# Performance work log

Hardware: AMD Instinct MI355X
Metric: run time of the kernel (lower is better)

The kernel has to match this reference:

```python
import jax, jax.numpy as jnp
import numpy as np

R = 16
ALPHA = 32.0
SCALING = ALPHA / R


def setup_inputs() -> dict:
    key = jax.random.key(0)
    ks = jax.random.split(key, 6)
    B, T, C, O, E = 16, 1500, 1024, 1024, 8
    x = jax.random.normal(ks[0], (B, T, C), dtype=jnp.float32)
    # gate weights per batch element (e.g. softmax-like, but module accepts any)
    w = jax.random.uniform(ks[1], (B, E), dtype=jnp.float32)
    W_base = jax.random.normal(ks[2], (O, C), dtype=jnp.float32) * 0.02
    b_base = jax.random.normal(ks[3], (O,), dtype=jnp.float32) * 0.02
    As = jax.random.normal(ks[4], (E, R, C), dtype=jnp.float32) * 0.02
    Bs = jax.random.normal(ks[5], (E, O, R), dtype=jnp.float32) * 0.02
    return {"x": x, "w": w, "W_base": W_base, "b_base": b_base, "As": As, "Bs": Bs}


def reference(x, w, W_base, b_base, As, Bs):
    # base linear: (B,T,C) @ (C,O) + b
    out = jnp.einsum('btc,oc->bto', x, W_base) + b_base
    # per-expert low-rank: h[b,t,e,r] = x[b,t,:] @ A_e^T
    h = jnp.einsum('btc,erc->bter', x, As)          # (B,T,E,R)
    # y[b,t,e,o] = h @ B_e^T ; gate-weighted sum over experts
    lora = jnp.einsum('bter,eor,be->bto', h, Bs, w)  # (B,T,O)
    return out + lora * SCALING
```

## Files before the change

kernel.cpp:

```cpp
#include <hip/hip_runtime.h>
#include <stdint.h>
#include <stddef.h>


#define B_ 16
#define T_ 1500
#define C_ 1024
#define O_ 1024
#define E_ 8
#define R_ 16
#define ER 128
#define KK 1152
#define BT 24000
#define NKT 18
#define SCALING 2.0f

typedef __bf16 bf16x8 __attribute__((ext_vector_type(8)));
typedef float f32x4 __attribute__((ext_vector_type(4)));
typedef unsigned short u16;
typedef u16 u16x8 __attribute__((ext_vector_type(8)));

__device__ inline u16 f2bf(float f) {
  union { float f; unsigned u; } v; v.f = f;
  unsigned u = v.u;
  u += 0x7fff + ((u >> 16) & 1);
  return (u16)(u >> 16);
}

#define GLL(gp, lp)                                                            \
  __builtin_amdgcn_global_load_lds(                                            \
      (const __attribute__((address_space(1))) void*)(gp),                     \
      (__attribute__((address_space(3))) void*)(lp), 16, 0, 0)

#define SBAR __builtin_amdgcn_sched_barrier(0)

__global__ __launch_bounds__(256) void prep_w(const float* __restrict__ Wb,
                                              const float* __restrict__ Bs,
                                              const float* __restrict__ As,
                                              u16* __restrict__ wp,
                                              u16* __restrict__ ap) {
  int idx = blockIdx.x * 256 + threadIdx.x;
  if (idx < O_ * KK) {
    int o = idx / KK;
    int k = idx - o * KK;
    float v;
    if (k < C_) {
      v = Wb[o * C_ + k];
    } else {
      int j = k - C_;
      v = Bs[((j >> 4) * O_ + o) * R_ + (j & 15)];
    }
    wp[idx] = f2bf(v);
  } else {
    int a = idx - O_ * KK;
    ap[a] = f2bf(As[a]);
  }
}

__global__ __launch_bounds__(256) void cvt(const float* __restrict__ x,
                                           u16* __restrict__ xp) {
  const int t0 = blockIdx.x * 256 + threadIdx.x;
#pragma unroll
  for (int u = 0; u < 6; ++u) {
    const int chunk = u * 512000 + t0;
    const int row = chunk >> 7;
    const int cc = (chunk & 127) * 8;
    const float4 v0 = *(const float4*)&x[(size_t)row * C_ + cc];
    const float4 v1 = *(const float4*)&x[(size_t)row * C_ + cc + 4];
    u16x8 o;
    o[0] = f2bf(v0.x); o[1] = f2bf(v0.y); o[2] = f2bf(v0.z); o[3] = f2bf(v0.w);
    o[4] = f2bf(v1.x); o[5] = f2bf(v1.y); o[6] = f2bf(v1.z); o[7] = f2bf(v1.w);
    *(u16x8*)&xp[(size_t)row * KK + cc] = o;
  }
}

__global__ __launch_bounds__(256) void h_gemm(const u16* __restrict__ xp,
                                              const u16* __restrict__ ab,
                                              const float* __restrict__ w,
                                              u16* __restrict__ xpo) {
  const int mt = blockIdx.x;
  const int tid = threadIdx.x, lane = tid & 63, wv = tid >> 6;
  const int wrow = wv & 1, wcol = wv >> 1, l15 = lane & 15, quad = lane >> 4;
  const int s7 = l15 & 7;

  __shared__ u16 lA[64 * 64];
  __shared__ u16 lB[128 * 64];

  const u16* gA = xp + (size_t)mt * 64 * KK;

  f32x4 acc[2][4];
#pragma unroll
  for (int i = 0; i < 2; ++i)
#pragma unroll
    for (int j = 0; j < 4; ++j) acc[i][j] = (f32x4){0.f, 0.f, 0.f, 0.f};

  int arow[2], ako[2], brow[4], bko[4];
#pragma unroll
  for (int c = 0; c < 2; ++c) {
    int idx = c * 256 + tid;
    arow[c] = idx >> 3;
    ako[c] = (((idx & 7) ^ (arow[c] & 7)) << 3);
  }
#pragma unroll
  for (int c = 0; c < 4; ++c) {
    int idx = c * 256 + tid;
    brow[c] = idx >> 3;
    bko[c] = (((idx & 7) ^ (brow[c] & 7)) << 3);
  }

  for (int kt = 0; kt < C_ / 64; ++kt) {
    const int k0 = kt * 64;
#pragma unroll
    for (int c = 0; c < 2; ++c)
      GLL(gA + (size_t)arow[c] * KK + k0 + ako[c], &lA[(c * 256 + tid) * 8]);
#pragma unroll
    for (int c = 0; c < 4; ++c)
      GLL(ab + brow[c] * C_ + k0 + bko[c], &lB[(c * 256 + tid) * 8]);
    __syncthreads();
#pragma unroll
    for (int kk = 0; kk < 2; ++kk) {
      const int ko = (((kk * 4 + quad) ^ s7) << 3);
      bf16x8 af[2], bfr[4];
#pragma unroll
      for (int i = 0; i < 2; ++i)
        af[i] = *(const bf16x8*)&lA[(wrow * 32 + i * 16 + l15) * 64 + ko];
#pragma unroll
      for (int j = 0; j < 4; ++j)
        bfr[j] = *(const bf16x8*)&lB[(wcol * 64 + j * 16 + l15) * 64 + ko];
#pragma unroll
      for (int i = 0; i < 2; ++i)
#pragma unroll
        for (int j = 0; j < 4; ++j)
          acc[i][j] = __builtin_amdgcn_mfma_f32_16x16x32_bf16(af[i], bfr[j], acc[i][j], 0, 0, 0);
    }
    __syncthreads();
  }

#pragma unroll
  for (int j = 0; j < 4; ++j) {
    const int col = wcol * 64 + j * 16 + l15;
    const int e = wcol * 4 + j;
#pragma unroll
    for (int i = 0; i < 2; ++i) {
#pragma unroll
      for (int rr = 0; rr < 4; ++rr) {
        const int row = mt * 64 + wrow * 32 + i * 16 + quad * 4 + rr;
        const int b = row / T_;
        xpo[(size_t)row * KK + C_ + col] = f2bf(acc[i][j][rr] * (SCALING * w[b * E_ + e]));
      }
    }
  }
}

__global__ __launch_bounds__(512, 2) void main_gemm(const u16* __restrict__ xp,
                                                    const u16* __restrict__ wp,
                                                    const float* __restrict__ bb,
                                                    float* __restrict__ out) {
  const int id = blockIdx.x;
  const int xcd = id & 7, win = id >> 3;
  const int g = (xcd < 4 ? xcd * 63 : 252 + (xcd - 4) * 62) + win;
  const int mt = g >> 2;
  const int nt = g & 3;
  const int tid = threadIdx.x, lane = tid & 63, wv = tid >> 6;
  const int wm = wv >> 2, wn = wv & 3, l15 = lane & 15, quad = lane >> 4;
  const int s7 = l15 & 7;
  const int ko0 = (quad ^ s7) << 3;
  const int ko1 = ((4 + quad) ^ s7) << 3;

  __shared__ u16 lA[2][192 * 64];
  __shared__ u16 lB[2][256 * 64];

  const u16* gA = xp + (size_t)mt * 192 * KK;
  const u16* gB = wp + (size_t)nt * 256 * KK;

  f32x4 acc[6][4];
#pragma unroll
  for (int i = 0; i < 6; ++i)
#pragma unroll
    for (int j = 0; j < 4; ++j) acc[i][j] = (f32x4){0.f, 0.f, 0.f, 0.f};

  const u16* pA[3];
  const u16* pB[4];
  int dA[3], dB[4];
#pragma unroll
  for (int c = 0; c < 3; ++c) {
    int idx = c * 512 + tid;
    int row = idx >> 3;
    pA[c] = gA + (size_t)row * KK + (((idx & 7) ^ (row & 7)) << 3);
    dA[c] = idx * 8;
  }
#pragma unroll
  for (int c = 0; c < 4; ++c) {
    int idx = c * 512 + tid;
    int row = idx >> 3;
    pB[c] = gB + (size_t)row * KK + (((idx & 7) ^ (row & 7)) << 3);
    dB[c] = idx * 8;
  }

#define ROWA(i) ((wm * 96 + (i) * 16 + l15) * 64)
#define ROWB(j) ((wn * 64 + (j) * 16 + l15) * 64)

#pragma unroll
  for (int c = 0; c < 3; ++c) GLL(pA[c], &lA[0][dA[c]]);
#pragma unroll
  for (int c = 0; c < 4; ++c) GLL(pB[c], &lB[0][dB[c]]);
#pragma unroll
  for (int c = 0; c < 3; ++c) GLL(pA[c] + 64, &lA[1][dA[c]]);
#pragma unroll
  for (int c = 0; c < 4; ++c) GLL(pB[c] + 64, &lB[1][dB[c]]);
  asm volatile("s_waitcnt vmcnt(7)" ::: "memory");
  SBAR;
  __builtin_amdgcn_s_barrier();
  SBAR;

  bf16x8 af0[3][2], af1[3][2], bfA[4][2], bfB[4][2];
#pragma unroll
  for (int i = 0; i < 3; ++i) {
    af0[i][0] = *(const bf16x8*)&lA[0][ROWA(i) + ko0];
    af0[i][1] = *(const bf16x8*)&lA[0][ROWA(i) + ko1];
  }
#pragma unroll
  for (int j = 0; j < 4; ++j) {
    bfA[j][0] = *(const bf16x8*)&lB[0][ROWB(j) + ko0];
    bfA[j][1] = *(const bf16x8*)&lB[0][ROWB(j) + ko1];
  }

#define TILE_BODY(T, CUR, BC, BN_)                                             \
  {                                                                            \
    const int t_ = (T);                                                        \
    _Pragma("unroll")                                                          \
    for (int i = 0; i < 3; ++i) {                                              \
      af1[i][0] = *(const bf16x8*)&lA[CUR][ROWA(i + 3) + ko0];                 \
      af1[i][1] = *(const bf16x8*)&lA[CUR][ROWA(i + 3) + ko1];                 \
    }                                                                          \
    __builtin_amdgcn_s_setprio(1);                                             \
    _Pragma("unroll")                                                          \
    for (int ks = 0; ks < 2; ++ks)                                             \
      _Pragma("unroll")                                                        \
      for (int i = 0; i < 3; ++i)                                              \
        _Pragma("unroll")                                                      \
        for (int j = 0; j < 4; ++j)                                            \
          acc[i][j] = __builtin_amdgcn_mfma_f32_16x16x32_bf16(                 \
              af0[i][ks], BC[j][ks], acc[i][j], 0, 0, 0);                      \
    __builtin_amdgcn_s_setprio(0);                                             \
    asm volatile("s_waitcnt lgkmcnt(0)" ::: "memory");                         \
    SBAR;                                                                      \
    __builtin_amdgcn_s_barrier();               \
    SBAR;                                                                      \
    if (t_ + 2 < NKT) {                                                        \
      const int k2 = (t_ + 2) * 64;                                            \
      _Pragma("unroll")                                                        \
      for (int c = 0; c < 3; ++c) GLL(pA[c] + k2, &lA[CUR][dA[c]]);            \
      _Pragma("unroll")                                                        \
      for (int c = 0; c < 4; ++c) GLL(pB[c] + k2, &lB[CUR][dB[c]]);            \
      asm volatile("s_waitcnt vmcnt(7)" ::: "memory");                         \
    } else {                                                                   \
      asm volatile("s_waitcnt vmcnt(0)" ::: "memory");                         \
    }                                                                          \
    SBAR;                                                                      \
    __builtin_amdgcn_s_barrier();     \
    SBAR;                                                                      \
    if (t_ + 1 < NKT) {                                                        \
      _Pragma("unroll")                                                        \
      for (int i = 0; i < 3; ++i) {                                            \
        af0[i][0] = *(const bf16x8*)&lA[CUR ^ 1][ROWA(i) + ko0];               \
        af0[i][1] = *(const bf16x8*)&lA[CUR ^ 1][ROWA(i) + ko1];               \
      }                                                                        \
      _Pragma("unroll")                                                        \
      for (int j = 0; j < 4; ++j) {                                            \
        BN_[j][0] = *(const bf16x8*)&lB[CUR ^ 1][ROWB(j) + ko0];               \
        BN_[j][1] = *(const bf16x8*)&lB[CUR ^ 1][ROWB(j) + ko1];               \
      }                                                                        \
    }                                                                          \
    __builtin_amdgcn_s_setprio(1);                                             \
    _Pragma("unroll")                                                          \
    for (int ks = 0; ks < 2; ++ks)                                             \
      _Pragma("unroll")                                                        \
      for (int i = 0; i < 3; ++i)                                              \
        _Pragma("unroll")                                                      \
        for (int j = 0; j < 4; ++j)                                            \
          acc[i + 3][j] = __builtin_amdgcn_mfma_f32_16x16x32_bf16(             \
              af1[i][ks], BC[j][ks], acc[i + 3][j], 0, 0, 0);                  \
    __builtin_amdgcn_s_setprio(0);                                             \
  }

  for (int tt = 0; tt < 9; ++tt) {
    TILE_BODY(2 * tt, 0, bfA, bfB)
    TILE_BODY(2 * tt + 1, 1, bfB, bfA)
  }
#undef TILE_BODY
#undef ROWA
#undef ROWB

#pragma unroll
  for (int j = 0; j < 4; ++j) {
    const int col = nt * 256 + wn * 64 + j * 16 + l15;
    const float bias = bb[col];
#pragma unroll
    for (int i = 0; i < 6; ++i) {
#pragma unroll
      for (int rr = 0; rr < 4; ++rr) {
        const int row = mt * 192 + wm * 96 + i * 16 + quad * 4 + rr;
        out[(size_t)row * O_ + col] = acc[i][j][rr] + bias;
      }
    }
  }
}

extern "C" void kernel_launch(void* const* d_in, const int* in_sizes, int n_in,
                              void* d_out, int out_size, void* d_ws, size_t ws_size,
                              hipStream_t stream) {
  const float* x = (const float*)d_in[0];
  const float* w = (const float*)d_in[1];
  const float* Wb = (const float*)d_in[2];
  const float* bb = (const float*)d_in[3];
  const float* As = (const float*)d_in[4];
  const float* Bs = (const float*)d_in[5];
  float* out = (float*)d_out;

  u16* xp = (u16*)d_ws;
  u16* wp = xp + (size_t)BT * KK;
  u16* ap = wp + (size_t)O_ * KK;

  prep_w<<<(O_ * KK + ER * C_) / 256, 256, 0, stream>>>(Wb, Bs, As, wp, ap);
  cvt<<<2000, 256, 0, stream>>>(x, xp);
  h_gemm<<<375, 256, 0, stream>>>(xp, ap, w, xp);
  main_gemm<<<500, 512, 0, stream>>>(xp, wp, bb, out);
}
```

Measured before the change: 275.4 us.

## Shrink main GEMM tile to 128 rows and use a triple-buffered LDS pipeline

The main GEMM tile shrinks from 192x256 to 128x256, which raises the grid from 500 to 752 blocks and adds a row guard on the output store. Shared memory is now triple-buffered: each k-step issues the global-to-LDS loads for two steps ahead, then reads this step's fragments in staged LDS reads interleaved with partial MFMA groups through lgkmcnt waits. The goal is to hide load latency with fewer barriers per step and to balance work across CUs. The cost is lower arithmetic intensity per block and more LDS use (about 144KB), which limits the kernel to one block per CU.

```diff
diff --git a/kernel.cpp b/kernel.cpp
--- a/kernel.cpp
+++ b/kernel.cpp
@@ -157,8 +157,7 @@
                                                     const float* __restrict__ bb,
                                                     float* __restrict__ out) {
   const int id = blockIdx.x;
-  const int xcd = id & 7, win = id >> 3;
-  const int g = (xcd < 4 ? xcd * 63 : 252 + (xcd - 4) * 62) + win;
+  const int g = (id & 7) * 94 + (id >> 3);
   const int mt = g >> 2;
   const int nt = g & 3;
   const int tid = threadIdx.x, lane = tid & 63, wv = tid >> 6;
@@ -167,23 +166,23 @@
   const int ko0 = (quad ^ s7) << 3;
   const int ko1 = ((4 + quad) ^ s7) << 3;
 
-  __shared__ u16 lA[2][192 * 64];
-  __shared__ u16 lB[2][256 * 64];
-
-  const u16* gA = xp + (size_t)mt * 192 * KK;
+  __shared__ u16 lA[3][128 * 64];
+  __shared__ u16 lB[3][256 * 64];
+
+  const u16* gA = xp + (size_t)mt * 128 * KK;
   const u16* gB = wp + (size_t)nt * 256 * KK;
 
-  f32x4 acc[6][4];
-#pragma unroll
-  for (int i = 0; i < 6; ++i)
+  f32x4 acc[4][4];
+#pragma unroll
+  for (int i = 0; i < 4; ++i)
 #pragma unroll
     for (int j = 0; j < 4; ++j) acc[i][j] = (f32x4){0.f, 0.f, 0.f, 0.f};
 
-  const u16* pA[3];
+  const u16* pA[2];
   const u16* pB[4];
-  int dA[3], dB[4];
-#pragma unroll
-  for (int c = 0; c < 3; ++c) {
+  int dA[2], dB[4];
+#pragma unroll
+  for (int c = 0; c < 2; ++c) {
     int idx = c * 512 + tid;
     int row = idx >> 3;
     pA[c] = gA + (size_t)row * KK + (((idx & 7) ^ (row & 7)) << 3);
@@ -197,96 +196,105 @@
     dB[c] = idx * 8;
   }
 
-#define ROWA(i) ((wm * 96 + (i) * 16 + l15) * 64)
+#define ROWA(i) ((wm * 64 + (i) * 16 + l15) * 64)
 #define ROWB(j) ((wn * 64 + (j) * 16 + l15) * 64)
 
 #pragma unroll
-  for (int c = 0; c < 3; ++c) GLL(pA[c], &lA[0][dA[c]]);
+  for (int c = 0; c < 2; ++c) GLL(pA[c], &lA[0][dA[c]]);
 #pragma unroll
   for (int c = 0; c < 4; ++c) GLL(pB[c], &lB[0][dB[c]]);
 #pragma unroll
-  for (int c = 0; c < 3; ++c) GLL(pA[c] + 64, &lA[1][dA[c]]);
+  for (int c = 0; c < 2; ++c) GLL(pA[c] + 64, &lA[1][dA[c]]);
 #pragma unroll
   for (int c = 0; c < 4; ++c) GLL(pB[c] + 64, &lB[1][dB[c]]);
-  asm volatile("s_waitcnt vmcnt(7)" ::: "memory");
-  SBAR;
-  __builtin_amdgcn_s_barrier();
-  SBAR;
-
-  bf16x8 af0[3][2], af1[3][2], bfA[4][2], bfB[4][2];
-#pragma unroll
-  for (int i = 0; i < 3; ++i) {
-    af0[i][0] = *(const bf16x8*)&lA[0][ROWA(i) + ko0];
-    af0[i][1] = *(const bf16x8*)&lA[0][ROWA(i) + ko1];
-  }
-#pragma unroll
-  for (int j = 0; j < 4; ++j) {
-    bfA[j][0] = *(const bf16x8*)&lB[0][ROWB(j) + ko0];
-    bfA[j][1] = *(const bf16x8*)&lB[0][ROWB(j) + ko1];
-  }
-
-#define TILE_BODY(T, CUR, BC, BN_)                                             \
+
+#define TILE_BODY(T, CUR, N2)                                                  \
   {                                                                            \
     const int t_ = (T);                                                        \
-    _Pragma("unroll")                                                          \
-    for (int i = 0; i < 3; ++i) {                                              \
-      af1[i][0] = *(const bf16x8*)&lA[CUR][ROWA(i + 3) + ko0];                 \
-      af1[i][1] = *(const bf16x8*)&lA[CUR][ROWA(i + 3) + ko1];                 \
-    }                                                                          \
-    __builtin_amdgcn_s_setprio(1);                                             \
-    _Pragma("unroll")                                                          \
-    for (int ks = 0; ks < 2; ++ks)                                             \
-      _Pragma("unroll")                                                        \
-      for (int i = 0; i < 3; ++i)                                              \
-        _Pragma("unroll")                                                      \
-        for (int j = 0; j < 4; ++j)                                            \
-          acc[i][j] = __builtin_amdgcn_mfma_f32_16x16x32_bf16(                 \
-              af0[i][ks], BC[j][ks], acc[i][j], 0, 0, 0);                      \
-    __builtin_amdgcn_s_setprio(0);                                             \
-    asm volatile("s_waitcnt lgkmcnt(0)" ::: "memory");                         \
-    SBAR;                                                                      \
-    __builtin_amdgcn_s_barrier();               \
+    if (t_ < NKT - 1) {                                                        \
+      asm volatile("s_waitcnt vmcnt(6)" ::: "memory");                         \
+    } else {                                                                   \
+      asm volatile("s_waitcnt vmcnt(0)" ::: "memory");                         \
+    }                                                                          \
+    SBAR;                                                                      \
+    __builtin_amdgcn_s_barrier();            \
     SBAR;                                                                      \
     if (t_ + 2 < NKT) {                                                        \
       const int k2 = (t_ + 2) * 64;                                            \
       _Pragma("unroll")                                                        \
-      for (int c = 0; c < 3; ++c) GLL(pA[c] + k2, &lA[CUR][dA[c]]);            \
-      _Pragma("unroll")                                                        \
-      for (int c = 0; c < 4; ++c) GLL(pB[c] + k2, &lB[CUR][dB[c]]);            \
-      asm volatile("s_waitcnt vmcnt(7)" ::: "memory");                         \
-    } else {                                                                   \
-      asm volatile("s_waitcnt vmcnt(0)" ::: "memory");                         \
-    }                                                                          \
-    SBAR;                                                                      \
-    __builtin_amdgcn_s_barrier();     \
-    SBAR;                                                                      \
-    if (t_ + 1 < NKT) {                                                        \
-      _Pragma("unroll")                                                        \
-      for (int i = 0; i < 3; ++i) {                                            \
-        af0[i][0] = *(const bf16x8*)&lA[CUR ^ 1][ROWA(i) + ko0];               \
-        af0[i][1] = *(const bf16x8*)&lA[CUR ^ 1][ROWA(i) + ko1];               \
-      }                                                                        \
-      _Pragma("unroll")                                                        \
-      for (int j = 0; j < 4; ++j) {                                            \
-        BN_[j][0] = *(const bf16x8*)&lB[CUR ^ 1][ROWB(j) + ko0];               \
-        BN_[j][1] = *(const bf16x8*)&lB[CUR ^ 1][ROWB(j) + ko1];               \
-      }                                                                        \
-    }                                                                          \
+      for (int c = 0; c < 2; ++c) GLL(pA[c] + k2, &lA[N2][dA[c]]);             \
+      _Pragma("unroll")                                                        \
+      for (int c = 0; c < 4; ++c) GLL(pB[c] + k2, &lB[N2][dB[c]]);             \
+    }                                                                          \
+    SBAR;                                                                      \
+    bf16x8 af[4][2], bfr[4][2];                                                \
+                              \
+    _Pragma("unroll")                                                          \
+    for (int i = 0; i < 2; ++i) {                                              \
+      af[i][0] = *(const bf16x8*)&lA[CUR][ROWA(i) + ko0];                      \
+      af[i][1] = *(const bf16x8*)&lA[CUR][ROWA(i) + ko1];                      \
+    }                                                                          \
+    _Pragma("unroll")                                                          \
+    for (int j = 0; j < 2; ++j) {                                              \
+      bfr[j][0] = *(const bf16x8*)&lB[CUR][ROWB(j) + ko0];                     \
+      bfr[j][1] = *(const bf16x8*)&lB[CUR][ROWB(j) + ko1];                     \
+    }                                                                          \
+    SBAR;                                                                      \
+                                            \
+    _Pragma("unroll")                                                          \
+    for (int i = 2; i < 4; ++i) {                                              \
+      af[i][0] = *(const bf16x8*)&lA[CUR][ROWA(i) + ko0];                      \
+      af[i][1] = *(const bf16x8*)&lA[CUR][ROWA(i) + ko1];                      \
+    }                                                                          \
+    SBAR;                                                                      \
+                                            \
+    _Pragma("unroll")                                                          \
+    for (int j = 2; j < 4; ++j) {                                              \
+      bfr[j][0] = *(const bf16x8*)&lB[CUR][ROWB(j) + ko0];                     \
+      bfr[j][1] = *(const bf16x8*)&lB[CUR][ROWB(j) + ko1];                     \
+    }                                                                          \
+    asm volatile("s_waitcnt lgkmcnt(8)" ::: "memory");            \
+    SBAR;                                                                      \
     __builtin_amdgcn_s_setprio(1);                                             \
     _Pragma("unroll")                                                          \
     for (int ks = 0; ks < 2; ++ks)                                             \
       _Pragma("unroll")                                                        \
-      for (int i = 0; i < 3; ++i)                                              \
+      for (int i = 0; i < 2; ++i)                                              \
         _Pragma("unroll")                                                      \
-        for (int j = 0; j < 4; ++j)                                            \
-          acc[i + 3][j] = __builtin_amdgcn_mfma_f32_16x16x32_bf16(             \
-              af1[i][ks], BC[j][ks], acc[i + 3][j], 0, 0, 0);                  \
+        for (int j = 0; j < 2; ++j)                                            \
+          acc[i][j] = __builtin_amdgcn_mfma_f32_16x16x32_bf16(                 \
+              af[i][ks], bfr[j][ks], acc[i][j], 0, 0, 0);                      \
     __builtin_amdgcn_s_setprio(0);                                             \
-  }
-
-  for (int tt = 0; tt < 9; ++tt) {
-    TILE_BODY(2 * tt, 0, bfA, bfB)
-    TILE_BODY(2 * tt + 1, 1, bfB, bfA)
+    asm volatile("s_waitcnt lgkmcnt(4)" ::: "memory");           \
+    SBAR;                                                                      \
+    __builtin_amdgcn_s_setprio(1);                                             \
+    _Pragma("unroll")                                                          \
+    for (int ks = 0; ks < 2; ++ks)                                             \
+      _Pragma("unroll")                                                        \
+      for (int i = 2; i < 4; ++i)                                              \
+        _Pragma("unroll")                                                      \
+        for (int j = 0; j < 2; ++j)                                            \
+          acc[i][j] = __builtin_amdgcn_mfma_f32_16x16x32_bf16(                 \
+              af[i][ks], bfr[j][ks], acc[i][j], 0, 0, 0);                      \
+    __builtin_amdgcn_s_setprio(0);                                             \
+    asm volatile("s_waitcnt lgkmcnt(0)" ::: "memory");           \
+    SBAR;                                                                      \
+    __builtin_amdgcn_s_setprio(1);                                             \
+    _Pragma("unroll")                                                          \
+    for (int ks = 0; ks < 2; ++ks)                                             \
+      _Pragma("unroll")                                                        \
+      for (int i = 0; i < 4; ++i)                                              \
+        _Pragma("unroll")                                                      \
+        for (int j = 2; j < 4; ++j)                                            \
+          acc[i][j] = __builtin_amdgcn_mfma_f32_16x16x32_bf16(                 \
+              af[i][ks], bfr[j][ks], acc[i][j], 0, 0, 0);                      \
+    __builtin_amdgcn_s_setprio(0);                                             \
+  }
+
+  for (int tt = 0; tt < 6; ++tt) {
+    TILE_BODY(3 * tt + 0, 0, 2)
+    TILE_BODY(3 * tt + 1, 1, 0)
+    TILE_BODY(3 * tt + 2, 2, 1)
   }
 #undef TILE_BODY
 #undef ROWA
@@ -297,11 +305,11 @@
     const int col = nt * 256 + wn * 64 + j * 16 + l15;
     const float bias = bb[col];
 #pragma unroll
-    for (int i = 0; i < 6; ++i) {
+    for (int i = 0; i < 4; ++i) {
 #pragma unroll
       for (int rr = 0; rr < 4; ++rr) {
-        const int row = mt * 192 + wm * 96 + i * 16 + quad * 4 + rr;
-        out[(size_t)row * O_ + col] = acc[i][j][rr] + bias;
+        const int row = mt * 128 + wm * 64 + i * 16 + quad * 4 + rr;
+        if (row < BT) out[(size_t)row * O_ + col] = acc[i][j][rr] + bias;
       }
     }
   }
@@ -325,5 +333,5 @@
   prep_w<<<(O_ * KK + ER * C_) / 256, 256, 0, stream>>>(Wb, Bs, As, wp, ap);
   cvt<<<2000, 256, 0, stream>>>(x, xp);
   h_gemm<<<375, 256, 0, stream>>>(xp, ap, w, xp);
-  main_gemm<<<500, 512, 0, stream>>>(xp, wp, bb, out);
-}
+  main_gemm<<<752, 512, 0, stream>>>(xp, wp, bb, out);
+}
```

Result: slower. 284.7 us (+3.4%).
